# Performance work log

Hardware: AMD Instinct MI355X
Metric: run time of the kernel (lower is better)

## Reference

```python
import jax, jax.numpy as jnp
import numpy as np

N_NODES = 50000
N_EDGES = 800000
D_IN = 128
D_HID = 128
N_CLASSES = 40


def gcn_conv(h, src, dst, W, b, n_nodes):
    """GCNConv: out = D^{-1/2} (A + I) D^{-1/2} (h @ W) + b, with self-loops."""
    h = h @ W  # [N, F_out]
    loop = jnp.arange(n_nodes, dtype=src.dtype)
    s = jnp.concatenate([src, loop])  # [E + N]
    d = jnp.concatenate([dst, loop])
    deg = jax.ops.segment_sum(jnp.ones_like(d, dtype=h.dtype), d, num_segments=n_nodes)
    dinv = jax.lax.rsqrt(jnp.maximum(deg, 1.0))  # deg >= 1 due to self-loops
    norm = dinv[s] * dinv[d]  # [E + N]
    msgs = h[s] * norm[:, None]  # gather: [E + N, F_out]
    out = jax.ops.segment_sum(msgs, d, num_segments=n_nodes)  # scatter-add
    return out + b


def setup_inputs() -> dict:
    key = jax.random.key(0)
    ks = jax.random.split(key, 12)
    x = jax.random.normal(ks[0], (N_NODES, D_IN), dtype=jnp.float32)
    edge_index = jax.random.randint(ks[1], (2, N_EDGES), 0, N_NODES, dtype=jnp.int64)
    def lin(k, fi, fo):
        s = 1.0 / np.sqrt(fi)
        return jax.random.uniform(k, (fi, fo), jnp.float32, -s, s)
    W_pre = lin(ks[2], D_IN, D_HID)
    b_pre = jnp.zeros((D_HID,), jnp.float32)
    W1 = lin(ks[3], D_HID, D_HID)
    b1 = jnp.zeros((D_HID,), jnp.float32)
    W2 = lin(ks[4], D_HID, D_HID)
    b2 = jnp.zeros((D_HID,), jnp.float32)
    W_post = lin(ks[5], D_HID, N_CLASSES)
    b_post = jnp.zeros((N_CLASSES,), jnp.float32)
    return {"x": x, "edge_index": edge_index, "W_pre": W_pre, "b_pre": b_pre,
            "W1": W1, "b1": b1, "W2": W2, "b2": b2,
            "W_post": W_post, "b_post": b_post}


def reference(x, edge_index, W_pre, b_pre, W1, b1, W2, b2, W_post, b_post):
    src, dst = edge_index[0], edge_index[1]
    n = x.shape[0]
    h = x @ W_pre + b_pre                      # pre-process MLP (Linear)
    h = jax.nn.relu(gcn_conv(h, src, dst, W1, b1, n))   # conv1 + act1
    h = jax.nn.relu(gcn_conv(h, src, dst, W2, b2, n))   # conv2 + act2
    return h @ W_post + b_post                 # post-process MLP (Linear)
```

## Files before the change

kernel.cpp:

```cpp
#include <hip/hip_runtime.h>

#define D 128

typedef short bfrag __attribute__((ext_vector_type(8)));
typedef float f32x4 __attribute__((ext_vector_type(4)));
typedef unsigned uint32;

__device__ inline unsigned short bf16_rne(float x) {
    unsigned u = __float_as_uint(x);
    return (unsigned short)((u + 0x7FFFu + ((u >> 16) & 1u)) >> 16);
}
__device__ inline float bf16_to_f(unsigned short h) {
    return __uint_as_float(((unsigned)h) << 16);
}
__device__ inline unsigned split2p(float x) {
    unsigned short hi = bf16_rne(x);
    unsigned short lo = bf16_rne(x - bf16_to_f(hi));
    return (unsigned)hi | ((unsigned)lo << 16);
}

__device__ inline void unpair_r(uint4 q0, uint4 q1, bfrag& ah, bfrag& al) {
    union { uint32 u[4]; bfrag b; } H, L;
    H.u[0] = __builtin_amdgcn_perm(q0.y, q0.x, 0x05040100u);
    H.u[1] = __builtin_amdgcn_perm(q0.w, q0.z, 0x05040100u);
    H.u[2] = __builtin_amdgcn_perm(q1.y, q1.x, 0x05040100u);
    H.u[3] = __builtin_amdgcn_perm(q1.w, q1.z, 0x05040100u);
    L.u[0] = __builtin_amdgcn_perm(q0.y, q0.x, 0x07060302u);
    L.u[1] = __builtin_amdgcn_perm(q0.w, q0.z, 0x07060302u);
    L.u[2] = __builtin_amdgcn_perm(q1.y, q1.x, 0x07060302u);
    L.u[3] = __builtin_amdgcn_perm(q1.w, q1.z, 0x07060302u);
    ah = H.b;
    al = L.b;
}

__device__ inline void split8_r(uint4 q0, uint4 q1, bfrag& ah, bfrag& al) {
    float v[8] = {__uint_as_float(q0.x), __uint_as_float(q0.y), __uint_as_float(q0.z), __uint_as_float(q0.w),
                  __uint_as_float(q1.x), __uint_as_float(q1.y), __uint_as_float(q1.z), __uint_as_float(q1.w)};
    union { unsigned short us[8]; bfrag b; } H, L;
    #pragma unroll
    for (int i = 0; i < 8; i++) {
        unsigned pr = split2p(v[i]);
        H.us[i] = (unsigned short)pr;
        L.us[i] = (unsigned short)(pr >> 16);
    }
    ah = H.b;
    al = L.b;
}

__global__ __launch_bounds__(256) void deg_raw(const unsigned* __restrict__ raw, int* __restrict__ deg,
                                               int* __restrict__ gmode, unsigned short* __restrict__ csr16,
                                               float* __restrict__ t_c, int E, int N, int csrCap4, int nRows) {
    __shared__ int smode;
    int gid = blockIdx.x * 256 + threadIdx.x;
    int gstride = gridDim.x * 256;
    int p0 = blockIdx.x * 1024;
    if (threadIdx.x < 64) {
        int p = p0 + threadIdx.x * 16;
        unsigned v = (p < E) ? raw[2 * p + 1] : 0u;
        unsigned long long any = __ballot(v != 0u);
        if (threadIdx.x == 0) smode = (any != 0ull) ? 1 : 0;
    }
    __syncthreads();
    int m = smode;
    if (blockIdx.x == 0 && threadIdx.x == 0) *gmode = m;
    unsigned short sent = (unsigned short)N;
    ushort4 s4 = make_ushort4(sent, sent, sent, sent);
    for (int i = gid; i < csrCap4; i += gstride) ((ushort4*)csr16)[i] = s4;
    int nSentF4 = 8 * (nRows - N) * 4;
    for (int i = gid; i < nSentF4; i += gstride) {
        int chunk = i / ((nRows - N) * 4);
        int rem = i % ((nRows - N) * 4);
        ((float4*)(t_c + (size_t)chunk * nRows * 16 + (size_t)N * 16))[rem] = make_float4(0.f, 0.f, 0.f, 0.f);
    }
    int pend = min(p0 + 1024, E);
    for (int p = p0 + threadIdx.x; p < pend; p += 256) {
        int d = m ? (int)raw[E + p] : (int)((const unsigned long long*)raw)[E + p];
        atomicAdd(&deg[d], 1);
    }
}

__global__ __launch_bounds__(256) void rank_block(const int* __restrict__ deg, float* __restrict__ dinv,
                                                  int* __restrict__ local_rank, int* __restrict__ hist_blk, int N) {
    __shared__ int h[256];
    int t = threadIdx.x;
    h[t] = 0;
    __syncthreads();
    int i = blockIdx.x * 256 + t;
    if (i < N) {
        int d = deg[i];
        dinv[i] = 1.0f / sqrtf((float)(d + 1));
        int b = min(d, 255);
        local_rank[i] = atomicAdd(&h[b], 1);
    }
    __syncthreads();
    hist_blk[blockIdx.x * 256 + t] = h[t];
}

__global__ __launch_bounds__(256) void scan_blocks(int* __restrict__ hist_blk, int* __restrict__ binbase,
                                                   int* __restrict__ ebase, int nblk) {
    int b = threadIdx.x;
    int sum = 0;
    int k = 0;
    for (; k + 8 <= nblk; k += 8) {
        int v[8];
        #pragma unroll
        for (int u = 0; u < 8; u++) v[u] = hist_blk[(k + u) * 256 + b];
        #pragma unroll
        for (int u = 0; u < 8; u++) { hist_blk[(k + u) * 256 + b] = sum; sum += v[u]; }
    }
    for (; k < nblk; k++) {
        int v = hist_blk[k * 256 + b];
        hist_blk[k * 256 + b] = sum;
        sum += v;
    }
    __shared__ int s[256], s2[256];
    int bp = (b + 3) & ~3;
    int c = sum, e = sum * bp;
    s[b] = c; s2[b] = e;
    __syncthreads();
    for (int off = 1; off < 256; off <<= 1) {
        int a0 = (b >= off) ? s[b - off] : 0;
        int a1 = (b >= off) ? s2[b - off] : 0;
        __syncthreads();
        s[b] += a0; s2[b] += a1;
        __syncthreads();
    }
    binbase[b] = s[b] - c;
    ebase[b] = s2[b] - e;
}

__global__ __launch_bounds__(256) void emit_perm(const int* __restrict__ deg, const float* __restrict__ dinv,
                                                 const int* __restrict__ local_rank, const int* __restrict__ hist_blk,
                                                 const int* __restrict__ binbase, const int* __restrict__ ebase,
                                                 int* __restrict__ tailcur, int* __restrict__ rowbeg,
                                                 int* __restrict__ cursor, uint4* __restrict__ meta, int N) {
    int i = blockIdx.x * 256 + threadIdx.x;
    if (i >= N) return;
    int d = deg[i];
    int b = min(d, 255);
    int dp = (d + 3) & ~3;
    int rib = hist_blk[blockIdx.x * 256 + b] + local_rank[i];
    int pos = binbase[b] + rib;
    int rb = (b < 255) ? (ebase[b] + rib * ((b + 3) & ~3)) : (ebase[255] + atomicAdd(tailcur, dp));
    rowbeg[i] = rb;
    cursor[i] = 0;
    meta[pos] = make_uint4((unsigned)rb, (unsigned)dp, __float_as_uint(dinv[i]), (unsigned)i);
}

__global__ __launch_bounds__(256) void fill_csr_raw(const unsigned* __restrict__ raw, const int* __restrict__ gmode,
                                                    const int* __restrict__ rowbeg, int* __restrict__ cursor,
                                                    unsigned short* __restrict__ csr16, int E) {
    int e = blockIdx.x * 256 + threadIdx.x;
    if (e >= E) return;
    int m = *gmode;
    int d = m ? (int)raw[E + e] : (int)((const unsigned long long*)raw)[E + e];
    int s = m ? (int)raw[e]     : (int)((const unsigned long long*)raw)[e];
    int pos = atomicAdd(&cursor[d], 1);
    csr16[rowbeg[d] + pos] = (unsigned short)s;
}

__global__ __launch_bounds__(256) void prep_w_all(const float* __restrict__ Wpre, const float* __restrict__ W1,
                                                  const float* __restrict__ W2, const float* __restrict__ Wpost,
                                                  unsigned short* __restrict__ preh, unsigned short* __restrict__ prel,
                                                  unsigned short* __restrict__ w1h, unsigned short* __restrict__ w1l,
                                                  unsigned short* __restrict__ w2h, unsigned short* __restrict__ w2l,
                                                  unsigned short* __restrict__ poh, unsigned short* __restrict__ pol) {
    int i = blockIdx.x * 256 + threadIdx.x;
    const float* W; unsigned short *wh, *wl; int idx, ncols;
    if (i < 16384)      { W = Wpre;  wh = preh; wl = prel; idx = i;         ncols = 128; }
    else if (i < 32768) { W = W1;    wh = w1h;  wl = w1l;  idx = i - 16384; ncols = 128; }
    else if (i < 49152) { W = W2;    wh = w2h;  wl = w2l;  idx = i - 32768; ncols = 128; }
    else if (i < 55296) { W = Wpost; wh = poh;  wl = pol;  idx = i - 49152; ncols = 40;  }
    else return;
    int n = idx >> 7, k = idx & 127;
    float v = (n < ncols) ? W[k * ncols + n] : 0.f;
    unsigned p = split2p(v);
    wh[idx] = (unsigned short)p;
    wl[idx] = (unsigned short)(p >> 16);
}

template<int NTILES, int EPI, int AFMT, int NW>
__global__ __launch_bounds__(NW * 64) void gemm_mfma(const void* __restrict__ Ap,
                                                     const unsigned short* __restrict__ Wth,
                                                     const unsigned short* __restrict__ Wtl,
                                                     const float* __restrict__ bias,
                                                     const float* __restrict__ dinv,
                                                     float* __restrict__ Cf,
                                                     uint32* __restrict__ Pout,
                                                     int nStrips, int N, int outW, int nRows) {
    int wave = threadIdx.x >> 6;
    int lane = threadIdx.x & 63;
    int l15 = lane & 15, lg = lane >> 4;
    int so, colbase;
    if (NW == 8) { so = wave >> 1; colbase = (wave & 1) * 64; }
    else         { so = wave;      colbase = 0; }
    size_t chunkStride = (size_t)nRows * 16;

    bfrag wh[4][NTILES], wl[4][NTILES];
    #pragma unroll
    for (int ks = 0; ks < 4; ks++)
        #pragma unroll
        for (int nt = 0; nt < NTILES; nt++) {
            size_t off = (size_t)(colbase + nt * 16 + l15) * D + ks * 32 + lg * 8;
            wh[ks][nt] = *(const bfrag*)(Wth + off);
            wl[ks][nt] = *(const bfrag*)(Wtl + off);
        }

    const int stride = gridDim.x * 4;
    int strip = blockIdx.x * 4 + so;
    if (strip >= nStrips) return;

    uint4 cur[8];
    auto loadraw = [&](int s, uint4* r) {
        int arow = min(s * 16 + l15, N - 1);
        const uint4* p = (const uint4*)Ap + (size_t)arow * 32 + lg * 2;
        #pragma unroll
        for (int ks = 0; ks < 4; ks++) {
            r[2 * ks]     = p[ks * 8];
            r[2 * ks + 1] = p[ks * 8 + 1];
        }
    };

    loadraw(strip, cur);
    while (true) {
        int next = strip + stride;
        bool has_next = next < nStrips;
        uint4 nxt[8];
        if (has_next) loadraw(next, nxt);

        bfrag ah[4], al[4];
        #pragma unroll
        for (int ks = 0; ks < 4; ks++) {
            if (AFMT == 0) unpair_r(cur[2 * ks], cur[2 * ks + 1], ah[ks], al[ks]);
            else           split8_r(cur[2 * ks], cur[2 * ks + 1], ah[ks], al[ks]);
        }
        f32x4 acc[NTILES];
        #pragma unroll
        for (int nt = 0; nt < NTILES; nt++) acc[nt] = (f32x4){0.f, 0.f, 0.f, 0.f};
        #pragma unroll
        for (int ks = 0; ks < 4; ks++) {
            #pragma unroll
            for (int nt = 0; nt < NTILES; nt++)
                acc[nt] = __builtin_amdgcn_mfma_f32_16x16x32_bf16(ah[ks], wh[ks][nt], acc[nt], 0, 0, 0);
            #pragma unroll
            for (int nt = 0; nt < NTILES; nt++)
                acc[nt] = __builtin_amdgcn_mfma_f32_16x16x32_bf16(ah[ks], wl[ks][nt], acc[nt], 0, 0, 0);
            #pragma unroll
            for (int nt = 0; nt < NTILES; nt++)
                acc[nt] = __builtin_amdgcn_mfma_f32_16x16x32_bf16(al[ks], wh[ks][nt], acc[nt], 0, 0, 0);
        }

        int row0 = strip * 16;
        float dv[4];
        if (EPI == 0) {
            #pragma unroll
            for (int r = 0; r < 4; r++) {
                int row = row0 + lg * 4 + r;
                dv[r] = (row < N) ? dinv[row] : 0.f;
            }
        }
        #pragma unroll
        for (int nt = 0; nt < NTILES; nt++) {
            int col = colbase + nt * 16 + l15;
            #pragma unroll
            for (int r = 0; r < 4; r++) {
                int row = row0 + lg * 4 + r;
                if (row >= N) continue;
                float v = acc[nt][r];
                if (EPI == 0) {
                    Cf[(size_t)(col >> 4) * chunkStride + (size_t)row * 16 + (col & 15)] = v * dv[r];
                } else if (EPI == 1) {
                    Pout[(size_t)row * D + col] = split2p(v + bias[col]);
                } else {
                    if (col < outW) Cf[(size_t)row * outW + col] = v + bias[col];
                }
            }
        }
        if (!has_next) break;
        #pragma unroll
        for (int i = 0; i < 8; i++) cur[i] = nxt[i];
        strip = next;
    }
}

__global__ __launch_bounds__(256) void gather_xcd(const unsigned short* __restrict__ csr16,
                                                  const uint4* __restrict__ meta,
                                                  const float* __restrict__ t_c, const float* __restrict__ bias,
                                                  uint32* __restrict__ Pout, int N, int nRows) {
    int chunk = blockIdx.x & 7;
    int k = (blockIdx.x >> 3) * 16 + (threadIdx.x >> 4);
    if (k >= N) return;
    uint4 m = meta[k];
    int beg = (int)m.x;
    int degp = (int)m.y;
    float di = __uint_as_float(m.z);
    int node = (int)m.w;
    int w = (threadIdx.x >> 2) & 3;
    int c = threadIdx.x & 3;
    const float* tc = t_c + (size_t)chunk * nRows * 16 + c * 4;
    float4 a0 = make_float4(0.f, 0.f, 0.f, 0.f);
    float4 a1 = make_float4(0.f, 0.f, 0.f, 0.f);
    float4 a2 = make_float4(0.f, 0.f, 0.f, 0.f);
    float4 a3 = make_float4(0.f, 0.f, 0.f, 0.f);
    int end = beg + degp;
    for (int j = beg + 4 * w; j < end; j += 16) {
        ushort4 o = *(const ushort4*)(csr16 + j);
        float4 v0 = *(const float4*)(tc + ((size_t)o.x << 4));
        float4 v1 = *(const float4*)(tc + ((size_t)o.y << 4));
        float4 v2 = *(const float4*)(tc + ((size_t)o.z << 4));
        float4 v3 = *(const float4*)(tc + ((size_t)o.w << 4));
        a0.x += v0.x; a0.y += v0.y; a0.z += v0.z; a0.w += v0.w;
        a1.x += v1.x; a1.y += v1.y; a1.z += v1.z; a1.w += v1.w;
        a2.x += v2.x; a2.y += v2.y; a2.z += v2.z; a2.w += v2.w;
        a3.x += v3.x; a3.y += v3.y; a3.z += v3.z; a3.w += v3.w;
    }
    a0.x += a1.x; a0.y += a1.y; a0.z += a1.z; a0.w += a1.w;
    a2.x += a3.x; a2.y += a3.y; a2.z += a3.z; a2.w += a3.w;
    a0.x += a2.x; a0.y += a2.y; a0.z += a2.z; a0.w += a2.w;
    a0.x += __shfl_xor(a0.x, 4); a0.y += __shfl_xor(a0.y, 4);
    a0.z += __shfl_xor(a0.z, 4); a0.w += __shfl_xor(a0.w, 4);
    a0.x += __shfl_xor(a0.x, 8); a0.y += __shfl_xor(a0.y, 8);
    a0.z += __shfl_xor(a0.z, 8); a0.w += __shfl_xor(a0.w, 8);
    if (w != 0) return;
    float4 tv = *(const float4*)(tc + (size_t)node * 16);
    int col0 = chunk * 16 + c * 4;
    float4 b = *((const float4*)bias + (col0 >> 2));
    float4 r;
    r.x = fmaxf(fmaf(di, a0.x + tv.x, b.x), 0.f);
    r.y = fmaxf(fmaf(di, a0.y + tv.y, b.y), 0.f);
    r.z = fmaxf(fmaf(di, a0.z + tv.z, b.z), 0.f);
    r.w = fmaxf(fmaf(di, a0.w + tv.w, b.w), 0.f);
    uint4 p;
    p.x = split2p(r.x); p.y = split2p(r.y); p.z = split2p(r.z); p.w = split2p(r.w);
    *(uint4*)(Pout + (size_t)node * D + col0) = p;
}

extern "C" void kernel_launch(void* const* d_in, const int* in_sizes, int n_in,
                              void* d_out, int out_size, void* d_ws, size_t ws_size,
                              hipStream_t stream) {
    const float* x      = (const float*)d_in[0];
    const unsigned* edges = (const unsigned*)d_in[1];
    const float* W_pre  = (const float*)d_in[2];
    const float* b_pre  = (const float*)d_in[3];
    const float* W1     = (const float*)d_in[4];
    const float* b1     = (const float*)d_in[5];
    const float* W2     = (const float*)d_in[6];
    const float* b2     = (const float*)d_in[7];
    const float* W_post = (const float*)d_in[8];
    const float* b_post = (const float*)d_in[9];
    float* out = (float*)d_out;

    const int N = in_sizes[0] / D;
    const int E = in_sizes[1] / 2;
    const int nStrips = (N + 15) / 16;
    const int Npad = nStrips * 16;
    const int nRows = Npad + 16;
    const int nBlk = (N + 255) / 256;
    const int csrCap = (E + 4 * N + 255) & ~255;

    char* ws = (char*)d_ws;
    size_t off = 0;
    auto alloc = [&](size_t bytes) { void* p = ws + off; off += (bytes + 255) & ~(size_t)255; return p; };
    uint32* pairA = (uint32*)alloc((size_t)Npad * D * 4);
    uint32* pairB = (uint32*)alloc((size_t)Npad * D * 4);
    float*  bufT  = (float*)alloc((size_t)8 * nRows * 16 * 4);
    float*  dinv    = (float*)alloc((size_t)N * 4);
    int*    deg     = (int*)alloc((size_t)N * 4);
    int*    rowbeg  = (int*)alloc((size_t)N * 4);
    unsigned short* csr16 = (unsigned short*)alloc((size_t)csrCap * 2);
    uint4*  meta    = (uint4*)alloc((size_t)N * 16);
    unsigned short* wpre_h  = (unsigned short*)alloc(128 * 128 * 2);
    unsigned short* wpre_l  = (unsigned short*)alloc(128 * 128 * 2);
    unsigned short* w1_h    = (unsigned short*)alloc(128 * 128 * 2);
    unsigned short* w1_l    = (unsigned short*)alloc(128 * 128 * 2);
    unsigned short* w2_h    = (unsigned short*)alloc(128 * 128 * 2);
    unsigned short* w2_l    = (unsigned short*)alloc(128 * 128 * 2);
    unsigned short* wpost_h = (unsigned short*)alloc(48 * 128 * 2);
    unsigned short* wpost_l = (unsigned short*)alloc(48 * 128 * 2);

    {
        char* t = (char*)bufT;
        size_t toff = 0;
        auto talloc = [&](size_t bytes) { void* p = t + toff; toff += (bytes + 255) & ~(size_t)255; return p; };
        int* cursor     = (int*)talloc((size_t)N * 4);
        int* local_rank = (int*)talloc((size_t)N * 4);
        int* hist_blk   = (int*)talloc((size_t)nBlk * 256 * 4);
        int* mode2      = (int*)talloc(256);
        int* binbase    = (int*)talloc(1024);
        int* ebase      = (int*)talloc(1024);
        int* gmode = mode2;
        int* tailcur = mode2 + 1;

        (void)hipMemsetAsync(mode2, 0, 8, stream);
        (void)hipMemsetAsync(deg, 0, (size_t)N * 4, stream);
        deg_raw<<<(E + 1023) / 1024, 256, 0, stream>>>(edges, deg, gmode, csr16, bufT, E, N, csrCap / 4, nRows);
        rank_block<<<nBlk, 256, 0, stream>>>(deg, dinv, local_rank, hist_blk, N);
        scan_blocks<<<1, 256, 0, stream>>>(hist_blk, binbase, ebase, nBlk);
        emit_perm<<<nBlk, 256, 0, stream>>>(deg, dinv, local_rank, hist_blk, binbase, ebase,
                                            tailcur, rowbeg, cursor, meta, N);
        fill_csr_raw<<<(E + 255) / 256, 256, 0, stream>>>(edges, gmode, rowbeg, cursor, csr16, E);
    }

    prep_w_all<<<216, 256, 0, stream>>>(W_pre, W1, W2, W_post,
                                        wpre_h, wpre_l, w1_h, w1_l, w2_h, w2_l, wpost_h, wpost_l);

    const int nGatherBlocks = ((N + 15) / 16) * 8;
    const int gemmGrid = 256;

    gemm_mfma<4, 1, 1, 8><<<gemmGrid, 512, 0, stream>>>(x, wpre_h, wpre_l, b_pre, nullptr, nullptr, pairB, nStrips, N, D, nRows);

    gemm_mfma<4, 0, 0, 8><<<gemmGrid, 512, 0, stream>>>(pairB, w1_h, w1_l, nullptr, dinv, bufT, nullptr, nStrips, N, D, nRows);
    gather_xcd<<<nGatherBlocks, 256, 0, stream>>>(csr16, meta, bufT, b1, pairA, N, nRows);

    gemm_mfma<4, 0, 0, 8><<<gemmGrid, 512, 0, stream>>>(pairA, w2_h, w2_l, nullptr, dinv, bufT, nullptr, nStrips, N, D, nRows);
    gather_xcd<<<nGatherBlocks, 256, 0, stream>>>(csr16, meta, bufT, b2, pairB, N, nRows);

    gemm_mfma<3, 2, 0, 4><<<gemmGrid, 256, 0, stream>>>(pairB, wpost_h, wpost_l, b_post, nullptr, out, nullptr, nStrips, N, 40, nRows);
}
```

Measured before the change: 297.6 us.

## Stage split weights in LDS for GEMMs and fold weight prep into degree kernel

The 128x128 GEMMs now load the hi/lo bf16 weight pairs into padded shared memory once per block and unpack them per MFMA, instead of holding all weight fragments in registers. This lowers register pressure and should raise occupancy. The grid grows from 256 to 391 blocks and the explicit next-strip prefetch is removed. Weight splitting is folded into the deg_raw kernel, dropping the separate prep_w_all launch, and weights are stored as packed uint32 pairs. Sentinel handling moves from N to Npad. The tradeoffs are extra LDS reads and unpack instructions inside the inner loop, and the loss of load/compute overlap from the removed prefetch.

```diff
diff --git a/kernel.cpp b/kernel.cpp
--- a/kernel.cpp
+++ b/kernel.cpp
@@ -49,7 +49,11 @@
 
 __global__ __launch_bounds__(256) void deg_raw(const unsigned* __restrict__ raw, int* __restrict__ deg,
                                                int* __restrict__ gmode, unsigned short* __restrict__ csr16,
-                                               float* __restrict__ t_c, int E, int N, int csrCap4, int nRows) {
+                                               float* __restrict__ t_c, int E, int Npad, int csrCap4, int nRows,
+                                               const float* __restrict__ Wpre, const float* __restrict__ W1,
+                                               const float* __restrict__ W2, const float* __restrict__ Wpost,
+                                               uint32* __restrict__ wpre_p, uint32* __restrict__ w1_p,
+                                               uint32* __restrict__ w2_p, uint32* __restrict__ wpost_p) {
     __shared__ int smode;
     int gid = blockIdx.x * 256 + threadIdx.x;
     int gstride = gridDim.x * 256;
@@ -63,14 +67,25 @@
     __syncthreads();
     int m = smode;
     if (blockIdx.x == 0 && threadIdx.x == 0) *gmode = m;
-    unsigned short sent = (unsigned short)N;
+    unsigned short sent = (unsigned short)Npad;
     ushort4 s4 = make_ushort4(sent, sent, sent, sent);
     for (int i = gid; i < csrCap4; i += gstride) ((ushort4*)csr16)[i] = s4;
-    int nSentF4 = 8 * (nRows - N) * 4;
+    int sentRows = nRows - Npad;
+    int nSentF4 = 8 * sentRows * 4;
     for (int i = gid; i < nSentF4; i += gstride) {
-        int chunk = i / ((nRows - N) * 4);
-        int rem = i % ((nRows - N) * 4);
-        ((float4*)(t_c + (size_t)chunk * nRows * 16 + (size_t)N * 16))[rem] = make_float4(0.f, 0.f, 0.f, 0.f);
+        int chunk = i / (sentRows * 4);
+        int rem = i % (sentRows * 4);
+        ((float4*)(t_c + (size_t)chunk * nRows * 16 + (size_t)Npad * 16))[rem] = make_float4(0.f, 0.f, 0.f, 0.f);
+    }
+    for (int i = gid; i < 55296; i += gstride) {
+        const float* W; uint32* wp; int idx, ncols;
+        if (i < 16384)      { W = Wpre;  wp = wpre_p;  idx = i;         ncols = 128; }
+        else if (i < 32768) { W = W1;    wp = w1_p;    idx = i - 16384; ncols = 128; }
+        else if (i < 49152) { W = W2;    wp = w2_p;    idx = i - 32768; ncols = 128; }
+        else                { W = Wpost; wp = wpost_p; idx = i - 49152; ncols = 40;  }
+        int n = idx >> 7, k = idx & 127;
+        float v = (n < ncols) ? W[k * ncols + n] : 0.f;
+        wp[idx] = split2p(v);
     }
     int pend = min(p0 + 1024, E);
     for (int p = p0 + threadIdx.x; p < pend; p += 256) {
@@ -159,127 +174,137 @@
     csr16[rowbeg[d] + pos] = (unsigned short)s;
 }
 
-__global__ __launch_bounds__(256) void prep_w_all(const float* __restrict__ Wpre, const float* __restrict__ W1,
-                                                  const float* __restrict__ W2, const float* __restrict__ Wpost,
-                                                  unsigned short* __restrict__ preh, unsigned short* __restrict__ prel,
-                                                  unsigned short* __restrict__ w1h, unsigned short* __restrict__ w1l,
-                                                  unsigned short* __restrict__ w2h, unsigned short* __restrict__ w2l,
-                                                  unsigned short* __restrict__ poh, unsigned short* __restrict__ pol) {
-    int i = blockIdx.x * 256 + threadIdx.x;
-    const float* W; unsigned short *wh, *wl; int idx, ncols;
-    if (i < 16384)      { W = Wpre;  wh = preh; wl = prel; idx = i;         ncols = 128; }
-    else if (i < 32768) { W = W1;    wh = w1h;  wl = w1l;  idx = i - 16384; ncols = 128; }
-    else if (i < 49152) { W = W2;    wh = w2h;  wl = w2l;  idx = i - 32768; ncols = 128; }
-    else if (i < 55296) { W = Wpost; wh = poh;  wl = pol;  idx = i - 49152; ncols = 40;  }
-    else return;
-    int n = idx >> 7, k = idx & 127;
-    float v = (n < ncols) ? W[k * ncols + n] : 0.f;
-    unsigned p = split2p(v);
-    wh[idx] = (unsigned short)p;
-    wl[idx] = (unsigned short)(p >> 16);
-}
-
-template<int NTILES, int EPI, int AFMT, int NW>
-__global__ __launch_bounds__(NW * 64) void gemm_mfma(const void* __restrict__ Ap,
-                                                     const unsigned short* __restrict__ Wth,
-                                                     const unsigned short* __restrict__ Wtl,
-                                                     const float* __restrict__ bias,
-                                                     const float* __restrict__ dinv,
-                                                     float* __restrict__ Cf,
-                                                     uint32* __restrict__ Pout,
-                                                     int nStrips, int N, int outW, int nRows) {
+template<int EPI, int AFMT>
+__global__ __launch_bounds__(512) void gemm_lds(const void* __restrict__ Ap,
+                                                const uint32* __restrict__ Wpair,
+                                                const float* __restrict__ bias,
+                                                const float* __restrict__ dinv,
+                                                float* __restrict__ Cf,
+                                                uint32* __restrict__ Pout,
+                                                int nStrips, int N, int nRows) {
+    __shared__ uint32 Wl[128 * 132];
+    int tid = threadIdx.x;
+    for (int i = tid; i < 16384; i += 512)
+        Wl[(i >> 7) * 132 + (i & 127)] = Wpair[i];
+    __syncthreads();
+
+    int wave = tid >> 6;
+    int lane = tid & 63;
+    int l15 = lane & 15, lg = lane >> 4;
+    int so = wave >> 1;
+    int colbase = (wave & 1) * 64;
+    size_t chunkStride = (size_t)nRows * 16;
+
+    const int stride = gridDim.x * 4;
+    for (int strip = blockIdx.x * 4 + so; strip < nStrips; strip += stride) {
+        int arow = min(strip * 16 + l15, N - 1);
+        uint4 cur[8];
+        const uint4* p = (const uint4*)Ap + (size_t)arow * 32 + lg * 2;
+        #pragma unroll
+        for (int ks = 0; ks < 4; ks++) {
+            cur[2 * ks]     = p[ks * 8];
+            cur[2 * ks + 1] = p[ks * 8 + 1];
+        }
+        bfrag ah[4], al[4];
+        #pragma unroll
+        for (int ks = 0; ks < 4; ks++) {
+            if (AFMT == 0) unpair_r(cur[2 * ks], cur[2 * ks + 1], ah[ks], al[ks]);
+            else           split8_r(cur[2 * ks], cur[2 * ks + 1], ah[ks], al[ks]);
+        }
+        f32x4 acc[4];
+        #pragma unroll
+        for (int nt = 0; nt < 4; nt++) acc[nt] = (f32x4){0.f, 0.f, 0.f, 0.f};
+        #pragma unroll
+        for (int ks = 0; ks < 4; ks++) {
+            #pragma unroll
+            for (int nt = 0; nt < 4; nt++) {
+                const uint32* wp = &Wl[(colbase + nt * 16 + l15) * 132 + ks * 32 + lg * 8];
+                uint4 w0 = *(const uint4*)wp;
+                uint4 w1 = *(const uint4*)(wp + 4);
+                bfrag wh, wl_;
+                unpair_r(w0, w1, wh, wl_);
+                acc[nt] = __builtin_amdgcn_mfma_f32_16x16x32_bf16(ah[ks], wh, acc[nt], 0, 0, 0);
+                acc[nt] = __builtin_amdgcn_mfma_f32_16x16x32_bf16(ah[ks], wl_, acc[nt], 0, 0, 0);
+                acc[nt] = __builtin_amdgcn_mfma_f32_16x16x32_bf16(al[ks], wh, acc[nt], 0, 0, 0);
+            }
+        }
+        int row0 = strip * 16;
+        if (EPI == 0) {
+            float dv[4];
+            #pragma unroll
+            for (int r = 0; r < 4; r++) dv[r] = dinv[min(row0 + lg * 4 + r, N - 1)];
+            #pragma unroll
+            for (int nt = 0; nt < 4; nt++) {
+                int col = colbase + nt * 16 + l15;
+                float* cbase = Cf + (size_t)(col >> 4) * chunkStride + (col & 15);
+                #pragma unroll
+                for (int r = 0; r < 4; r++)
+                    cbase[(size_t)(row0 + lg * 4 + r) * 16] = acc[nt][r] * dv[r];
+            }
+        } else {
+            #pragma unroll
+            for (int nt = 0; nt < 4; nt++) {
+                int col = colbase + nt * 16 + l15;
+                float bv = bias[col];
+                #pragma unroll
+                for (int r = 0; r < 4; r++)
+                    Pout[(size_t)(row0 + lg * 4 + r) * D + col] = split2p(acc[nt][r] + bv);
+            }
+        }
+    }
+}
+
+__global__ __launch_bounds__(256) void gemm_post(const uint32* __restrict__ P,
+                                                 const uint32* __restrict__ Wpair,
+                                                 const float* __restrict__ bias,
+                                                 float* __restrict__ Cf,
+                                                 int nStrips, int N, int outW) {
     int wave = threadIdx.x >> 6;
     int lane = threadIdx.x & 63;
     int l15 = lane & 15, lg = lane >> 4;
-    int so, colbase;
-    if (NW == 8) { so = wave >> 1; colbase = (wave & 1) * 64; }
-    else         { so = wave;      colbase = 0; }
-    size_t chunkStride = (size_t)nRows * 16;
-
-    bfrag wh[4][NTILES], wl[4][NTILES];
+
+    bfrag wh[4][3], wl[4][3];
     #pragma unroll
     for (int ks = 0; ks < 4; ks++)
         #pragma unroll
-        for (int nt = 0; nt < NTILES; nt++) {
-            size_t off = (size_t)(colbase + nt * 16 + l15) * D + ks * 32 + lg * 8;
-            wh[ks][nt] = *(const bfrag*)(Wth + off);
-            wl[ks][nt] = *(const bfrag*)(Wtl + off);
+        for (int nt = 0; nt < 3; nt++) {
+            const uint32* wp = Wpair + (size_t)(nt * 16 + l15) * D + ks * 32 + lg * 8;
+            uint4 w0 = *(const uint4*)wp;
+            uint4 w1 = *(const uint4*)(wp + 4);
+            unpair_r(w0, w1, wh[ks][nt], wl[ks][nt]);
         }
 
     const int stride = gridDim.x * 4;
-    int strip = blockIdx.x * 4 + so;
-    if (strip >= nStrips) return;
-
-    uint4 cur[8];
-    auto loadraw = [&](int s, uint4* r) {
-        int arow = min(s * 16 + l15, N - 1);
-        const uint4* p = (const uint4*)Ap + (size_t)arow * 32 + lg * 2;
+    for (int strip = blockIdx.x * 4 + wave; strip < nStrips; strip += stride) {
+        int arow = min(strip * 16 + l15, N - 1);
+        bfrag ah[4], al[4];
         #pragma unroll
         for (int ks = 0; ks < 4; ks++) {
-            r[2 * ks]     = p[ks * 8];
-            r[2 * ks + 1] = p[ks * 8 + 1];
-        }
-    };
-
-    loadraw(strip, cur);
-    while (true) {
-        int next = strip + stride;
-        bool has_next = next < nStrips;
-        uint4 nxt[8];
-        if (has_next) loadraw(next, nxt);
-
-        bfrag ah[4], al[4];
-        #pragma unroll
-        for (int ks = 0; ks < 4; ks++) {
-            if (AFMT == 0) unpair_r(cur[2 * ks], cur[2 * ks + 1], ah[ks], al[ks]);
-            else           split8_r(cur[2 * ks], cur[2 * ks + 1], ah[ks], al[ks]);
-        }
-        f32x4 acc[NTILES];
-        #pragma unroll
-        for (int nt = 0; nt < NTILES; nt++) acc[nt] = (f32x4){0.f, 0.f, 0.f, 0.f};
-        #pragma unroll
-        for (int ks = 0; ks < 4; ks++) {
-            #pragma unroll
-            for (int nt = 0; nt < NTILES; nt++)
+            const uint4* p = (const uint4*)P + (size_t)arow * 32 + lg * 2;
+            unpair_r(p[ks * 8], p[ks * 8 + 1], ah[ks], al[ks]);
+        }
+        f32x4 acc[3];
+        #pragma unroll
+        for (int nt = 0; nt < 3; nt++) acc[nt] = (f32x4){0.f, 0.f, 0.f, 0.f};
+        #pragma unroll
+        for (int ks = 0; ks < 4; ks++)
+            #pragma unroll
+            for (int nt = 0; nt < 3; nt++) {
                 acc[nt] = __builtin_amdgcn_mfma_f32_16x16x32_bf16(ah[ks], wh[ks][nt], acc[nt], 0, 0, 0);
-            #pragma unroll
-            for (int nt = 0; nt < NTILES; nt++)
                 acc[nt] = __builtin_amdgcn_mfma_f32_16x16x32_bf16(ah[ks], wl[ks][nt], acc[nt], 0, 0, 0);
-            #pragma unroll
-            for (int nt = 0; nt < NTILES; nt++)
                 acc[nt] = __builtin_amdgcn_mfma_f32_16x16x32_bf16(al[ks], wh[ks][nt], acc[nt], 0, 0, 0);
-        }
-
+            }
         int row0 = strip * 16;
-        float dv[4];
-        if (EPI == 0) {
+        #pragma unroll
+        for (int nt = 0; nt < 3; nt++) {
+            int col = nt * 16 + l15;
             #pragma unroll
             for (int r = 0; r < 4; r++) {
                 int row = row0 + lg * 4 + r;
-                dv[r] = (row < N) ? dinv[row] : 0.f;
+                if (row < N && col < outW)
+                    Cf[(size_t)row * outW + col] = acc[nt][r] + bias[col];
             }
         }
-        #pragma unroll
-        for (int nt = 0; nt < NTILES; nt++) {
-            int col = colbase + nt * 16 + l15;
-            #pragma unroll
-            for (int r = 0; r < 4; r++) {
-                int row = row0 + lg * 4 + r;
-                if (row >= N) continue;
-                float v = acc[nt][r];
-                if (EPI == 0) {
-                    Cf[(size_t)(col >> 4) * chunkStride + (size_t)row * 16 + (col & 15)] = v * dv[r];
-                } else if (EPI == 1) {
-                    Pout[(size_t)row * D + col] = split2p(v + bias[col]);
-                } else {
-                    if (col < outW) Cf[(size_t)row * outW + col] = v + bias[col];
-                }
-            }
-        }
-        if (!has_next) break;
-        #pragma unroll
-        for (int i = 0; i < 8; i++) cur[i] = nxt[i];
-        strip = next;
     }
 }
 
@@ -369,14 +394,10 @@
     int*    rowbeg  = (int*)alloc((size_t)N * 4);
     unsigned short* csr16 = (unsigned short*)alloc((size_t)csrCap * 2);
     uint4*  meta    = (uint4*)alloc((size_t)N * 16);
-    unsigned short* wpre_h  = (unsigned short*)alloc(128 * 128 * 2);
-    unsigned short* wpre_l  = (unsigned short*)alloc(128 * 128 * 2);
-    unsigned short* w1_h    = (unsigned short*)alloc(128 * 128 * 2);
-    unsigned short* w1_l    = (unsigned short*)alloc(128 * 128 * 2);
-    unsigned short* w2_h    = (unsigned short*)alloc(128 * 128 * 2);
-    unsigned short* w2_l    = (unsigned short*)alloc(128 * 128 * 2);
-    unsigned short* wpost_h = (unsigned short*)alloc(48 * 128 * 2);
-    unsigned short* wpost_l = (unsigned short*)alloc(48 * 128 * 2);
+    uint32* wpre_p  = (uint32*)alloc(16384 * 4);
+    uint32* w1_p    = (uint32*)alloc(16384 * 4);
+    uint32* w2_p    = (uint32*)alloc(16384 * 4);
+    uint32* wpost_p = (uint32*)alloc(6144 * 4);
 
     {
         char* t = (char*)bufT;
@@ -393,7 +414,8 @@
 
         (void)hipMemsetAsync(mode2, 0, 8, stream);
         (void)hipMemsetAsync(deg, 0, (size_t)N * 4, stream);
-        deg_raw<<<(E + 1023) / 1024, 256, 0, stream>>>(edges, deg, gmode, csr16, bufT, E, N, csrCap / 4, nRows);
+        deg_raw<<<(E + 1023) / 1024, 256, 0, stream>>>(edges, deg, gmode, csr16, bufT, E, Npad, csrCap / 4, nRows,
+                                                       W_pre, W1, W2, W_post, wpre_p, w1_p, w2_p, wpost_p);
         rank_block<<<nBlk, 256, 0, stream>>>(deg, dinv, local_rank, hist_blk, N);
         scan_blocks<<<1, 256, 0, stream>>>(hist_blk, binbase, ebase, nBlk);
         emit_perm<<<nBlk, 256, 0, stream>>>(deg, dinv, local_rank, hist_blk, binbase, ebase,
@@ -401,19 +423,16 @@
         fill_csr_raw<<<(E + 255) / 256, 256, 0, stream>>>(edges, gmode, rowbeg, cursor, csr16, E);
     }
 
-    prep_w_all<<<216, 256, 0, stream>>>(W_pre, W1, W2, W_post,
-                                        wpre_h, wpre_l, w1_h, w1_l, w2_h, w2_l, wpost_h, wpost_l);
-
     const int nGatherBlocks = ((N + 15) / 16) * 8;
-    const int gemmGrid = 256;
-
-    gemm_mfma<4, 1, 1, 8><<<gemmGrid, 512, 0, stream>>>(x, wpre_h, wpre_l, b_pre, nullptr, nullptr, pairB, nStrips, N, D, nRows);
-
-    gemm_mfma<4, 0, 0, 8><<<gemmGrid, 512, 0, stream>>>(pairB, w1_h, w1_l, nullptr, dinv, bufT, nullptr, nStrips, N, D, nRows);
+    const int gemmGrid = 391;
+
+    gemm_lds<1, 1><<<gemmGrid, 512, 0, stream>>>(x, wpre_p, b_pre, nullptr, nullptr, pairB, nStrips, N, nRows);
+
+    gemm_lds<0, 0><<<gemmGrid, 512, 0, stream>>>(pairB, w1_p, nullptr, dinv, bufT, nullptr, nStrips, N, nRows);
     gather_xcd<<<nGatherBlocks, 256, 0, stream>>>(csr16, meta, bufT, b1, pairA, N, nRows);
 
-    gemm_mfma<4, 0, 0, 8><<<gemmGrid, 512, 0, stream>>>(pairA, w2_h, w2_l, nullptr, dinv, bufT, nullptr, nStrips, N, D, nRows);
+    gemm_lds<0, 0><<<gemmGrid, 512, 0, stream>>>(pairA, w2_p, nullptr, dinv, bufT, nullptr, nStrips, N, nRows);
     gather_xcd<<<nGatherBlocks, 256, 0, stream>>>(csr16, meta, bufT, b2, pairB, N, nRows);
 
-    gemm_mfma<3, 2, 0, 4><<<gemmGrid, 256, 0, stream>>>(pairB, wpost_h, wpost_l, b_post, nullptr, out, nullptr, nStrips, N, 40, nRows);
-}
+    gemm_post<<<256, 256, 0, stream>>>(pairB, wpost_p, b_post, out, nStrips, N, 40);
+}
```

After: 267.3 us. 1.11x faster.
